# Kernel optimization log

Measured on AMD Instinct MI355X. Metric: run time of the kernel, lower is better.

Reference implementation:

```python
import jax, jax.numpy as jnp
import numpy as np

N_HEADS = 64
N_KV = 8
HEAD_DIM = 128
HIDDEN = 8192
BATCH = 32
PAD_LEN = 2048  # nearest_32(start_pos + 1) with start_pos = 2047


def setup_inputs() -> dict:
    key = jax.random.key(0)
    ks = jax.random.split(key, 8)
    w = 0.02
    return {
        "x": jax.random.normal(ks[0], (BATCH, 1, HIDDEN), jnp.float32),
        "wq": jax.random.normal(ks[1], (HIDDEN, N_HEADS * HEAD_DIM), jnp.float32) * w,
        "wk": jax.random.normal(ks[2], (HIDDEN, N_KV * HEAD_DIM), jnp.float32) * w,
        "wv": jax.random.normal(ks[3], (HIDDEN, N_KV * HEAD_DIM), jnp.float32) * w,
        "wo": jax.random.normal(ks[4], (N_HEADS * HEAD_DIM, HIDDEN), jnp.float32) * w,
        "rot_mat": jax.random.normal(ks[5], (HEAD_DIM, HEAD_DIM), jnp.float32) * w,
        "k_cache": jax.random.normal(ks[6], (BATCH, N_KV, PAD_LEN, HEAD_DIM), jnp.float32),
        "v_cache": jax.random.normal(ks[7], (BATCH, N_KV, PAD_LEN, HEAD_DIM), jnp.float32),
        "start_pos": 2047,
    }


def reference(x, wq, wk, wv, wo, rot_mat, k_cache, v_cache, start_pos):
    B = x.shape[0]
    L = k_cache.shape[2]  # padded past length (nearest_32(start_pos+1))
    scale = 1.0 / np.sqrt(HEAD_DIM).astype(np.float32)

    xt = x[:, 0]  # [B, HIDDEN], seq_len == 1 (decode)
    # QKV projections + rotary applied via explicit matmul with rot_mat
    q = (xt @ wq).reshape(B, N_HEADS, HEAD_DIM) @ rot_mat      # [B, nH, d]
    k_new = (xt @ wk).reshape(B, N_KV, HEAD_DIM) @ rot_mat     # [B, nKV, d]
    v_new = (xt @ wv).reshape(B, N_KV, HEAD_DIM)               # [B, nKV, d]

    # in-place KV cache update at current position
    keys = k_cache.at[:, :, start_pos].set(k_new)              # [B, nKV, L, d]
    vals = v_cache.at[:, :, start_pos].set(v_new)

    # grouped (multi-query) attention: 8 q-heads per kv-head
    qg = q.reshape(B, N_KV, N_HEADS // N_KV, HEAD_DIM)         # [B, nKV, g, d]
    scores = jnp.einsum("bkgd,bkld->bkgl", qg, keys) * scale   # [B, nKV, g, L]
    # padded causal mask: positions beyond start_pos are masked with finfo.min
    mask = jnp.where(jnp.arange(L) > start_pos,
                     jnp.finfo(scores.dtype).min, 0.0).astype(scores.dtype)
    attn = jax.nn.softmax(scores + mask, axis=-1)
    out = jnp.einsum("bkgl,bkld->bkgd", attn, vals)            # [B, nKV, g, d]
    out = out.reshape(B, N_HEADS * HEAD_DIM) @ wo              # dense out-proj
    return out[:, None, :]                                     # [B, 1, HIDDEN]
```

## Files before the change

### kernel.cpp

```cpp
#include <hip/hip_runtime.h>
#include <hip/hip_bf16.h>

#define HIDDEN 8192
#define NHEADS 64
#define NKV 8
#define HD 128
#define BATCH 32
#define PADLEN 2048
#define NCHUNK 4
#define CHUNKLEN 512

using bf16x8 = __attribute__((ext_vector_type(8))) short;
using f32x4 = __attribute__((ext_vector_type(4))) float;

__device__ __forceinline__ void gld16(const float* g, float* l) {
    __builtin_amdgcn_global_load_lds(
        (const __attribute__((address_space(1))) void*)g,
        (__attribute__((address_space(3))) void*)l,
        16, 0, 0);
}

__device__ __forceinline__ float readlane_f(float v, int lane) {
    return __uint_as_float(__builtin_amdgcn_readlane(__float_as_uint(v), lane));
}

__device__ __forceinline__ short f2bf(float f) {
    unsigned u = __float_as_uint(f);
    u += 0x7fff + ((u >> 16) & 1);
    return (short)(u >> 16);
}
__device__ __forceinline__ float bf2f(short s) {
    return __uint_as_float(((unsigned)(unsigned short)s) << 16);
}

__global__ __launch_bounds__(256) void cvt_split(const float* __restrict__ in,
                                                 short* __restrict__ hi,
                                                 short* __restrict__ lo, int n4) {
    int i = blockIdx.x * 256 + threadIdx.x;
    if (i >= n4) return;
    float4 v = ((const float4*)in)[i];
    short4 h, l;
    h.x = f2bf(v.x); l.x = f2bf(v.x - bf2f(h.x));
    h.y = f2bf(v.y); l.y = f2bf(v.y - bf2f(h.y));
    h.z = f2bf(v.z); l.z = f2bf(v.z - bf2f(h.z));
    h.w = f2bf(v.w); l.w = f2bf(v.w - bf2f(h.w));
    ((short4*)hi)[i] = h;
    ((short4*)lo)[i] = l;
}

#define KC 256
#define QSEC 262144
#define KSEC 294912
#define QKV_STRIDE 327680
#define NSPLIT 16
#define KSLICE 512

__global__ __launch_bounds__(256) void gemm_mfma(
        const short* __restrict__ xhi, const short* __restrict__ xlo,
        const float* __restrict__ W0, const float* __restrict__ W1,
        const float* __restrict__ W2, float* __restrict__ P, size_t pstride) {
    const int tid = threadIdx.x;
    const int wv = tid >> 6, ln = tid & 63;
    const int cb = blockIdx.x, kb = blockIdx.y;

    const float* W; int N2; size_t so; int nbase;
    if (cb < 32)      { W = W0; N2 = 8192; so = 0;    nbase = cb * 256; }
    else if (cb < 36) { W = W1; N2 = 1024; so = QSEC; nbase = (cb - 32) * 256; }
    else              { W = W2; N2 = 1024; so = KSEC; nbase = (cb - 36) * 256; }

    const int n0 = nbase + wv * 64;
    const int lrow = ln & 15;
    const int kgrp = ln >> 4;

    f32x4 acc[2][4];
#pragma unroll
    for (int mt = 0; mt < 2; ++mt)
#pragma unroll
        for (int nt = 0; nt < 4; ++nt)
            acc[mt][nt] = (f32x4){0.f, 0.f, 0.f, 0.f};

    const int k0 = kb * KSLICE;
    for (int kk = 0; kk < KSLICE; kk += 32) {
        const int kbase = k0 + kk + kgrp * 8;
        bf16x8 a0h = *(const bf16x8*)(xhi + (size_t)lrow * HIDDEN + kbase);
        bf16x8 a0l = *(const bf16x8*)(xlo + (size_t)lrow * HIDDEN + kbase);
        bf16x8 a1h = *(const bf16x8*)(xhi + (size_t)(lrow + 16) * HIDDEN + kbase);
        bf16x8 a1l = *(const bf16x8*)(xlo + (size_t)(lrow + 16) * HIDDEN + kbase);
#pragma unroll
        for (int nt = 0; nt < 4; ++nt) {
            const float* wp = W + (size_t)kbase * N2 + (n0 + nt * 16 + lrow);
            bf16x8 bh, bl;
#pragma unroll
            for (int j = 0; j < 8; ++j) {
                float wf = wp[(size_t)j * N2];
                short h = f2bf(wf);
                bh[j] = h;
                bl[j] = f2bf(wf - bf2f(h));
            }
            acc[0][nt] = __builtin_amdgcn_mfma_f32_16x16x32_bf16(a0h, bh, acc[0][nt], 0, 0, 0);
            acc[1][nt] = __builtin_amdgcn_mfma_f32_16x16x32_bf16(a1h, bh, acc[1][nt], 0, 0, 0);
            acc[0][nt] = __builtin_amdgcn_mfma_f32_16x16x32_bf16(a0l, bh, acc[0][nt], 0, 0, 0);
            acc[1][nt] = __builtin_amdgcn_mfma_f32_16x16x32_bf16(a1l, bh, acc[1][nt], 0, 0, 0);
            acc[0][nt] = __builtin_amdgcn_mfma_f32_16x16x32_bf16(a0h, bl, acc[0][nt], 0, 0, 0);
            acc[1][nt] = __builtin_amdgcn_mfma_f32_16x16x32_bf16(a1h, bl, acc[1][nt], 0, 0, 0);
        }
    }

    float* pb = P + (size_t)kb * pstride + so;
#pragma unroll
    for (int mt = 0; mt < 2; ++mt)
#pragma unroll
        for (int nt = 0; nt < 4; ++nt)
#pragma unroll
            for (int r = 0; r < 4; ++r) {
                int row = mt * 16 + kgrp * 4 + r;
                pb[(size_t)row * N2 + n0 + nt * 16 + lrow] = acc[mt][nt][r];
            }
}

__global__ __launch_bounds__(256) void reduce_split(const float* __restrict__ P,
                                                    float* __restrict__ out,
                                                    int nelem, size_t pstride) {
    int i = (blockIdx.x * 256 + threadIdx.x) * 4;
    if (i >= nelem) return;
    float4 a = *(const float4*)(P + i);
#pragma unroll 4
    for (int s = 1; s < NSPLIT; ++s) {
        float4 b = *(const float4*)(P + (size_t)s * pstride + i);
        a.x += b.x; a.y += b.y; a.z += b.z; a.w += b.w;
    }
    *(float4*)(out + i) = a;
}

#define RROWS 16
__global__ __launch_bounds__(128) void rotary_all(const float* __restrict__ qin,
                                                  const float* __restrict__ kin,
                                                  const float* __restrict__ rot,
                                                  float* __restrict__ qout,
                                                  float* __restrict__ kout) {
    __shared__ float rows[RROWS][HD];
    const int tid = threadIdx.x;
    const int row0 = blockIdx.x * RROWS;

    for (int i = tid; i < RROWS * (HD / 4); i += 128) {
        int r = i >> 5;
        int d4 = i & 31;
        int gr = row0 + r;
        const float* src = (gr < BATCH * NHEADS)
                               ? (qin + (size_t)gr * HD)
                               : (kin + (size_t)(gr - BATCH * NHEADS) * HD);
        *(float4*)&rows[r][d4 * 4] = *(const float4*)(src + d4 * 4);
    }
    __syncthreads();

    float acc[RROWS];
#pragma unroll
    for (int r = 0; r < RROWS; ++r) acc[r] = 0.f;

    for (int d4 = 0; d4 < HD; d4 += 4) {
        float r0 = rot[(size_t)(d4 + 0) * HD + tid];
        float r1 = rot[(size_t)(d4 + 1) * HD + tid];
        float r2 = rot[(size_t)(d4 + 2) * HD + tid];
        float r3 = rot[(size_t)(d4 + 3) * HD + tid];
#pragma unroll
        for (int r = 0; r < RROWS; ++r) {
            float4 xv = *(const float4*)&rows[r][d4];
            acc[r] = fmaf(xv.x, r0, acc[r]);
            acc[r] = fmaf(xv.y, r1, acc[r]);
            acc[r] = fmaf(xv.z, r2, acc[r]);
            acc[r] = fmaf(xv.w, r3, acc[r]);
        }
    }
#pragma unroll
    for (int r = 0; r < RROWS; ++r) {
        int gr = row0 + r;
        float* dst = (gr < BATCH * NHEADS)
                         ? (qout + (size_t)gr * HD)
                         : (kout + (size_t)(gr - BATCH * NHEADS) * HD);
        dst[tid] = acc[r];
    }
}

#define TILE 16
#define NBUF 4
__global__ __launch_bounds__(512, 4) void attn_decode(
        const float* __restrict__ qr, const float* __restrict__ kr,
        const float* __restrict__ vnew, const float* __restrict__ kcache,
        const float* __restrict__ vcache, const int* __restrict__ sp_ptr,
        float* __restrict__ part_acc, float* __restrict__ part_md) {
    __shared__ float4 kt[NBUF][TILE][32];
    __shared__ float4 vt[NBUF][TILE][32];

    const int tid = threadIdx.x;
    const int wv = tid >> 6, ln = tid & 63;
    const int row = ln & 15, qd = ln >> 4;
    const int dslot = ln & 31, hh = ln >> 5;
    const int chunk = blockIdx.x >> 8;
    const int b  = (blockIdx.x >> 3) & 31;
    const int kv = blockIdx.x & 7;
    const int chunk0 = chunk * CHUNKLEN;
    const int sp = sp_ptr[0];
    const float scale = 0.08838834764831845f;
    const int bh = b * NHEADS + kv * 8 + wv;

    const float* kbase = kcache + (size_t)(b * NKV + kv) * PADLEN * HD;
    const float* vbase = vcache + (size_t)(b * NKV + kv) * PADLEN * HD;
    const float* knew  = kr   + (size_t)(b * NKV + kv) * HD;
    const float* vnw   = vnew + (size_t)(b * NKV + kv) * HD;

    float4 qreg[8];
    {
        const float4* qsrc = (const float4*)(qr + (size_t)bh * HD) + qd * 8;
#pragma unroll
        for (int i = 0; i < 8; ++i) qreg[i] = qsrc[i];
    }

    const int sr  = wv * 2 + (ln >> 5);
    const int sj  = ln & 31;
    const int sjk = sj ^ (sr & 7);

    float m_run = -1e30f, dsum = 0.f;
    float4 acc = make_float4(0.f, 0.f, 0.f, 0.f);

    int valid = sp + 1 - chunk0;
    int nt = valid <= 0 ? 0 : (valid + TILE - 1) >> 4;
    if (nt > CHUNKLEN / TILE) nt = CHUNKLEN / TILE;

    auto stage = [&](int ts, int slot) {
        const int gl = chunk0 + (ts << 4) + sr;
        const float* krow = (gl == sp) ? knew : (kbase + (size_t)gl * HD);
        const float* vrow = (gl == sp) ? vnw  : (vbase + (size_t)gl * HD);
        gld16(krow + (sjk << 2), (float*)&kt[slot][0][0] + wv * 256);
        gld16(vrow + (sj  << 2), (float*)&vt[slot][0][0] + wv * 256);
    };

    auto compute = [&](int t) {
        const float4 (*kt_)[32] = kt[t & 3];
        const float4 (*vt_)[32] = vt[t & 3];
        float sh = 0.f;
#pragma unroll
        for (int jj = 0; jj < 8; ++jj) {
            float4 kk = kt_[row][(qd * 8 + jj) ^ (row & 7)];
            float4 qq = qreg[jj];
            sh = fmaf(qq.x, kk.x, sh);
            sh = fmaf(qq.y, kk.y, sh);
            sh = fmaf(qq.z, kk.z, sh);
            sh = fmaf(qq.w, kk.w, sh);
        }
        sh += __shfl_xor(sh, 16);
        sh += __shfl_xor(sh, 32);
        float s0 = sh * scale;
        const int l0 = chunk0 + (t << 4) + row;
        const bool dead = l0 > sp;
        if (dead) s0 = -1e30f;

        float mt = s0;
        mt = fmaxf(mt, __shfl_xor(mt, 1));
        mt = fmaxf(mt, __shfl_xor(mt, 2));
        mt = fmaxf(mt, __shfl_xor(mt, 4));
        mt = fmaxf(mt, __shfl_xor(mt, 8));
        float mnew = fmaxf(m_run, mt);
        float f = __expf(m_run - mnew);
        float p0 = dead ? 0.f : __expf(s0 - mnew);
        m_run = mnew;
        dsum = dsum * f + p0;
        acc.x *= f; acc.y *= f; acc.z *= f; acc.w *= f;

#pragma unroll
        for (int i = 0; i < 8; ++i) {
            float4 vv = vt_[hh * 8 + i][dslot];
            float pa = readlane_f(p0, i);
            float pb = readlane_f(p0, 8 + i);
            float pr = hh ? pb : pa;
            acc.x = fmaf(pr, vv.x, acc.x);
            acc.y = fmaf(pr, vv.y, acc.y);
            acc.z = fmaf(pr, vv.z, acc.z);
            acc.w = fmaf(pr, vv.w, acc.w);
        }
    };

    if (nt > 0) {
        stage(0, 0);
        stage(nt > 1 ? 1 : 0, 1);
        for (int t = 0; t < nt; ++t) {
            int ts = t + 2 < nt ? t + 2 : nt - 1;
            stage(ts, (t + 2) & 3);
            asm volatile("s_waitcnt vmcnt(4)" ::: "memory");
            __builtin_amdgcn_s_barrier();
            compute(t);
        }
    }

    acc.x += __shfl_xor(acc.x, 32);
    acc.y += __shfl_xor(acc.y, 32);
    acc.z += __shfl_xor(acc.z, 32);
    acc.w += __shfl_xor(acc.w, 32);
    float dd = dsum;
    dd += __shfl_xor(dd, 1);
    dd += __shfl_xor(dd, 2);
    dd += __shfl_xor(dd, 4);
    dd += __shfl_xor(dd, 8);

    if (hh == 0)
        *(float4*)(part_acc + ((size_t)chunk * (BATCH * NHEADS) + bh) * HD + dslot * 4) = acc;
    if (ln == 0) {
        float2 md = make_float2(m_run, dd);
        *(float2*)(part_md + ((size_t)chunk * (BATCH * NHEADS) + bh) * 2) = md;
    }
}

__global__ __launch_bounds__(128) void attn_combine(const float* __restrict__ part_acc,
                                                    const float* __restrict__ part_md,
                                                    float* __restrict__ attn_out) {
    const int bh = blockIdx.x;
    const int d = threadIdx.x;
    float m[NCHUNK], dd[NCHUNK];
    float M = -1e30f;
#pragma unroll
    for (int c = 0; c < NCHUNK; ++c) {
        m[c]  = part_md[((size_t)c * (BATCH * NHEADS) + bh) * 2];
        dd[c] = part_md[((size_t)c * (BATCH * NHEADS) + bh) * 2 + 1];
        M = fmaxf(M, m[c]);
    }
    float D = 0.f, o = 0.f;
#pragma unroll
    for (int c = 0; c < NCHUNK; ++c) {
        float w = __expf(m[c] - M);
        D += dd[c] * w;
        o += part_acc[((size_t)c * (BATCH * NHEADS) + bh) * HD + d] * w;
    }
    attn_out[(size_t)bh * HD + d] = o / D;
}

extern "C" void kernel_launch(void* const* d_in, const int* in_sizes, int n_in,
                              void* d_out, int out_size, void* d_ws, size_t ws_size,
                              hipStream_t stream) {
    const float* x   = (const float*)d_in[0];
    const float* wq  = (const float*)d_in[1];
    const float* wk  = (const float*)d_in[2];
    const float* wv  = (const float*)d_in[3];
    const float* wo  = (const float*)d_in[4];
    const float* rot = (const float*)d_in[5];
    const float* kc  = (const float*)d_in[6];
    const float* vc  = (const float*)d_in[7];
    const int*   sp  = (const int*)d_in[8];
    float* out = (float*)d_out;

    float* ws = (float*)d_ws;
    float* qkv_buf  = ws;
    float* q_buf    = qkv_buf;
    float* k_buf    = qkv_buf + QSEC;
    float* v_buf    = qkv_buf + KSEC;
    float* qr_buf   = ws + 327680;
    float* kr_buf   = ws + 589824;
    float* attn_buf = ws + 622592;
    short* xhi      = (short*)(ws + 884736);
    short* xlo      = (short*)(ws + 884736 + 131072);
    short* ahi      = (short*)(ws + 884736 + 262144);
    short* alo      = (short*)(ws + 884736 + 393216);
    float* P        = ws + 884736 + 524288;
    float* part_acc = P;
    float* part_md  = P + 1048576;

    cvt_split<<<(QSEC / 4 + 255) / 256, 256, 0, stream>>>(x, xhi, xlo, QSEC / 4);
    gemm_mfma<<<dim3(40, NSPLIT), 256, 0, stream>>>(xhi, xlo, wq, wk, wv, P, QKV_STRIDE);
    reduce_split<<<(QKV_STRIDE / 4 + 255) / 256, 256, 0, stream>>>(
        P, qkv_buf, QKV_STRIDE, QKV_STRIDE);

    rotary_all<<<(BATCH * NHEADS + BATCH * NKV) / RROWS, 128, 0, stream>>>(
        q_buf, k_buf, rot, qr_buf, kr_buf);

    attn_decode<<<NCHUNK * BATCH * NKV, 512, 0, stream>>>(
        qr_buf, kr_buf, v_buf, kc, vc, sp, part_acc, part_md);
    attn_combine<<<BATCH * NHEADS, 128, 0, stream>>>(part_acc, part_md, attn_buf);

    cvt_split<<<(QSEC / 4 + 255) / 256, 256, 0, stream>>>(attn_buf, ahi, alo, QSEC / 4);
    gemm_mfma<<<dim3(32, NSPLIT), 256, 0, stream>>>(ahi, alo, wo, wo, wo, P, QSEC);
    reduce_split<<<(QSEC / 4 + 255) / 256, 256, 0, stream>>>(P, out, QSEC, QSEC);
}
```

Before: 303.3 us.

## Halve GEMM column tile per block and software-pipeline weight loads

Each wave of the split-K MFMA GEMM now covers 32 output columns instead of 64, and the grid doubles (80 and 64 column blocks), giving twice as many workgroups for the weight-streaming projections. The K loop is fully unrolled and double-buffered in registers, so the next step's weight and activation loads are issued before the current step's bf16 split and MFMAs. The aim is more memory-level parallelism and latency hiding on the bandwidth-bound fp32 weight reads. The cost is more register use and re-reading the activation rows from twice as many blocks.

```diff
diff --git a/kernel.cpp b/kernel.cpp
--- a/kernel.cpp
+++ b/kernel.cpp
@@ -48,7 +48,6 @@
     ((short4*)lo)[i] = l;
 }
 
-#define KC 256
 #define QSEC 262144
 #define KSEC 294912
 #define QKV_STRIDE 327680
@@ -64,58 +63,85 @@
     const int cb = blockIdx.x, kb = blockIdx.y;
 
     const float* W; int N2; size_t so; int nbase;
-    if (cb < 32)      { W = W0; N2 = 8192; so = 0;    nbase = cb * 256; }
-    else if (cb < 36) { W = W1; N2 = 1024; so = QSEC; nbase = (cb - 32) * 256; }
-    else              { W = W2; N2 = 1024; so = KSEC; nbase = (cb - 36) * 256; }
-
-    const int n0 = nbase + wv * 64;
+    if (cb < 64)      { W = W0; N2 = 8192; so = 0;    nbase = cb * 128; }
+    else if (cb < 72) { W = W1; N2 = 1024; so = QSEC; nbase = (cb - 64) * 128; }
+    else              { W = W2; N2 = 1024; so = KSEC; nbase = (cb - 72) * 128; }
+
+    const int n0 = nbase + wv * 32;
     const int lrow = ln & 15;
     const int kgrp = ln >> 4;
-
-    f32x4 acc[2][4];
-#pragma unroll
-    for (int mt = 0; mt < 2; ++mt)
-#pragma unroll
-        for (int nt = 0; nt < 4; ++nt)
-            acc[mt][nt] = (f32x4){0.f, 0.f, 0.f, 0.f};
-
     const int k0 = kb * KSLICE;
-    for (int kk = 0; kk < KSLICE; kk += 32) {
-        const int kbase = k0 + kk + kgrp * 8;
-        bf16x8 a0h = *(const bf16x8*)(xhi + (size_t)lrow * HIDDEN + kbase);
-        bf16x8 a0l = *(const bf16x8*)(xlo + (size_t)lrow * HIDDEN + kbase);
-        bf16x8 a1h = *(const bf16x8*)(xhi + (size_t)(lrow + 16) * HIDDEN + kbase);
-        bf16x8 a1l = *(const bf16x8*)(xlo + (size_t)(lrow + 16) * HIDDEN + kbase);
-#pragma unroll
-        for (int nt = 0; nt < 4; ++nt) {
-            const float* wp = W + (size_t)kbase * N2 + (n0 + nt * 16 + lrow);
-            bf16x8 bh, bl;
-#pragma unroll
-            for (int j = 0; j < 8; ++j) {
-                float wf = wp[(size_t)j * N2];
-                short h = f2bf(wf);
-                bh[j] = h;
-                bl[j] = f2bf(wf - bf2f(h));
-            }
-            acc[0][nt] = __builtin_amdgcn_mfma_f32_16x16x32_bf16(a0h, bh, acc[0][nt], 0, 0, 0);
-            acc[1][nt] = __builtin_amdgcn_mfma_f32_16x16x32_bf16(a1h, bh, acc[1][nt], 0, 0, 0);
-            acc[0][nt] = __builtin_amdgcn_mfma_f32_16x16x32_bf16(a0l, bh, acc[0][nt], 0, 0, 0);
-            acc[1][nt] = __builtin_amdgcn_mfma_f32_16x16x32_bf16(a1l, bh, acc[1][nt], 0, 0, 0);
-            acc[0][nt] = __builtin_amdgcn_mfma_f32_16x16x32_bf16(a0h, bl, acc[0][nt], 0, 0, 0);
-            acc[1][nt] = __builtin_amdgcn_mfma_f32_16x16x32_bf16(a1h, bl, acc[1][nt], 0, 0, 0);
-        }
-    }
+
+    const float* wp0 = W + (size_t)(k0 + kgrp * 8) * N2 + (n0 + lrow);
+    const float* wp1 = wp0 + 16;
+    const short* xh0 = xhi + (size_t)lrow * HIDDEN + k0 + kgrp * 8;
+    const short* xl0 = xlo + (size_t)lrow * HIDDEN + k0 + kgrp * 8;
+    const short* xh1 = xh0 + (size_t)16 * HIDDEN;
+    const short* xl1 = xl0 + (size_t)16 * HIDDEN;
+
+    f32x4 acc00 = {0.f,0.f,0.f,0.f}, acc01 = {0.f,0.f,0.f,0.f};
+    f32x4 acc10 = {0.f,0.f,0.f,0.f}, acc11 = {0.f,0.f,0.f,0.f};
+
+    float c0[8], c1[8], pb0[8], pb1[8];
+    bf16x8 A0h, A0l, A1h, A1l, N0h, N0l, N1h, N1l;
+
+    auto loadB = [&](int kk, float (&b0)[8], float (&b1)[8]) {
+#pragma unroll
+        for (int j = 0; j < 8; ++j) {
+            b0[j] = wp0[(size_t)(kk + j) * N2];
+            b1[j] = wp1[(size_t)(kk + j) * N2];
+        }
+    };
+    auto loadA = [&](int kk, bf16x8& h0, bf16x8& l0, bf16x8& h1, bf16x8& l1) {
+        h0 = *(const bf16x8*)(xh0 + kk);
+        l0 = *(const bf16x8*)(xl0 + kk);
+        h1 = *(const bf16x8*)(xh1 + kk);
+        l1 = *(const bf16x8*)(xl1 + kk);
+    };
+    auto domfma = [&](float (&b0)[8], float (&b1)[8],
+                      bf16x8 ah0, bf16x8 al0, bf16x8 ah1, bf16x8 al1) {
+        bf16x8 bh0, bl0, bh1, bl1;
+#pragma unroll
+        for (int j = 0; j < 8; ++j) {
+            short h0 = f2bf(b0[j]); bh0[j] = h0; bl0[j] = f2bf(b0[j] - bf2f(h0));
+            short h1 = f2bf(b1[j]); bh1[j] = h1; bl1[j] = f2bf(b1[j] - bf2f(h1));
+        }
+        acc00 = __builtin_amdgcn_mfma_f32_16x16x32_bf16(ah0, bh0, acc00, 0, 0, 0);
+        acc10 = __builtin_amdgcn_mfma_f32_16x16x32_bf16(ah1, bh0, acc10, 0, 0, 0);
+        acc01 = __builtin_amdgcn_mfma_f32_16x16x32_bf16(ah0, bh1, acc01, 0, 0, 0);
+        acc11 = __builtin_amdgcn_mfma_f32_16x16x32_bf16(ah1, bh1, acc11, 0, 0, 0);
+        acc00 = __builtin_amdgcn_mfma_f32_16x16x32_bf16(al0, bh0, acc00, 0, 0, 0);
+        acc10 = __builtin_amdgcn_mfma_f32_16x16x32_bf16(al1, bh0, acc10, 0, 0, 0);
+        acc01 = __builtin_amdgcn_mfma_f32_16x16x32_bf16(al0, bh1, acc01, 0, 0, 0);
+        acc11 = __builtin_amdgcn_mfma_f32_16x16x32_bf16(al1, bh1, acc11, 0, 0, 0);
+        acc00 = __builtin_amdgcn_mfma_f32_16x16x32_bf16(ah0, bl0, acc00, 0, 0, 0);
+        acc10 = __builtin_amdgcn_mfma_f32_16x16x32_bf16(ah1, bl0, acc10, 0, 0, 0);
+        acc01 = __builtin_amdgcn_mfma_f32_16x16x32_bf16(ah0, bl1, acc01, 0, 0, 0);
+        acc11 = __builtin_amdgcn_mfma_f32_16x16x32_bf16(ah1, bl1, acc11, 0, 0, 0);
+    };
+
+    loadB(0, c0, c1);
+    loadA(0, A0h, A0l, A1h, A1l);
+#pragma unroll
+    for (int kk = 0; kk < KSLICE - 32; kk += 32) {
+        loadB(kk + 32, pb0, pb1);
+        loadA(kk + 32, N0h, N0l, N1h, N1l);
+        domfma(c0, c1, A0h, A0l, A1h, A1l);
+#pragma unroll
+        for (int j = 0; j < 8; ++j) { c0[j] = pb0[j]; c1[j] = pb1[j]; }
+        A0h = N0h; A0l = N0l; A1h = N1h; A1l = N1l;
+    }
+    domfma(c0, c1, A0h, A0l, A1h, A1l);
 
     float* pb = P + (size_t)kb * pstride + so;
 #pragma unroll
-    for (int mt = 0; mt < 2; ++mt)
-#pragma unroll
-        for (int nt = 0; nt < 4; ++nt)
-#pragma unroll
-            for (int r = 0; r < 4; ++r) {
-                int row = mt * 16 + kgrp * 4 + r;
-                pb[(size_t)row * N2 + n0 + nt * 16 + lrow] = acc[mt][nt][r];
-            }
+    for (int r = 0; r < 4; ++r) {
+        int row0 = kgrp * 4 + r;
+        pb[(size_t)row0 * N2 + n0 + lrow]            = acc00[r];
+        pb[(size_t)row0 * N2 + n0 + 16 + lrow]       = acc01[r];
+        pb[(size_t)(row0 + 16) * N2 + n0 + lrow]      = acc10[r];
+        pb[(size_t)(row0 + 16) * N2 + n0 + 16 + lrow] = acc11[r];
+    }
 }
 
 __global__ __launch_bounds__(256) void reduce_split(const float* __restrict__ P,
@@ -363,7 +389,7 @@
     float* part_md  = P + 1048576;
 
     cvt_split<<<(QSEC / 4 + 255) / 256, 256, 0, stream>>>(x, xhi, xlo, QSEC / 4);
-    gemm_mfma<<<dim3(40, NSPLIT), 256, 0, stream>>>(xhi, xlo, wq, wk, wv, P, QKV_STRIDE);
+    gemm_mfma<<<dim3(80, NSPLIT), 256, 0, stream>>>(xhi, xlo, wq, wk, wv, P, QKV_STRIDE);
     reduce_split<<<(QKV_STRIDE / 4 + 255) / 256, 256, 0, stream>>>(
         P, qkv_buf, QKV_STRIDE, QKV_STRIDE);
 
@@ -375,6 +401,6 @@
     attn_combine<<<BATCH * NHEADS, 128, 0, stream>>>(part_acc, part_md, attn_buf);
 
     cvt_split<<<(QSEC / 4 + 255) / 256, 256, 0, stream>>>(attn_buf, ahi, alo, QSEC / 4);
-    gemm_mfma<<<dim3(32, NSPLIT), 256, 0, stream>>>(ahi, alo, wo, wo, wo, P, QSEC);
+    gemm_mfma<<<dim3(64, NSPLIT), 256, 0, stream>>>(ahi, alo, wo, wo, wo, P, QSEC);
     reduce_split<<<(QSEC / 4 + 255) / 256, 256, 0, stream>>>(P, out, QSEC, QSEC);
 }
```

Result: no change. 302.5 us (-0.3%).
